# Optimization experiments

Hardware: AMD Instinct MI355X
Metric: run time of the kernel (lower is better)

Reference implementation:

```python
import jax, jax.numpy as jnp
import numpy as np

DIM = 1024
N_SRC = 4096
N_TGT = 4096


def setup_inputs() -> dict:
    key = jax.random.key(0)
    ks = jax.random.split(key, 7)
    scale = 1.0 / np.sqrt(DIM)
    return {
        "source": jax.random.normal(ks[0], (N_SRC, DIM), dtype=jnp.float32),
        "target": jax.random.normal(ks[1], (N_TGT, DIM), dtype=jnp.float32),
        "W_src": jax.random.uniform(ks[2], (DIM, DIM), minval=-scale, maxval=scale, dtype=jnp.float32),
        "b_src": jax.random.uniform(ks[3], (DIM,), minval=-scale, maxval=scale, dtype=jnp.float32),
        "W_tgt": jax.random.uniform(ks[4], (DIM, DIM), minval=-scale, maxval=scale, dtype=jnp.float32),
        "b_tgt": jax.random.uniform(ks[5], (DIM,), minval=-scale, maxval=scale, dtype=jnp.float32),
        "temperature": jnp.array(1.0, dtype=jnp.float32),
    }


def reference(source, target, W_src, b_src, W_tgt, b_tgt, temperature):
    # Linear projections (torch Linear: x @ W.T + b)
    sp = source @ W_src.T + b_src            # [N, d]
    tp = target @ W_tgt.T + b_tgt            # [M, d]
    sq_s = jnp.sum(sp * sp, axis=-1, keepdims=True)   # [N, 1]
    sq_t = jnp.sum(tp * tp, axis=-1)                  # [M]
    d2 = sq_s + sq_t[None, :] - 2.0 * (sp @ tp.T)     # [N, M]
    cost = jnp.sqrt(jnp.maximum(d2, 0.0))
    # Softmin-style kernel, row-normalized over target entries
    K = jnp.exp(-cost / temperature)
    K = K / jnp.sum(K, axis=1, keepdims=True)
    aligned_source = K @ target                       # [N, d]
    return aligned_source, K
```

## Files before the change

kernel.cpp:

```cpp
#include <hip/hip_runtime.h>
#include <stdint.h>

#define DIM  1024
#define NSRC 4096
#define NTGT 4096

typedef __bf16 bf16_t;
typedef bf16_t bf16x8 __attribute__((ext_vector_type(8)));
typedef float  fx4    __attribute__((ext_vector_type(4)));

static __device__ __forceinline__ unsigned short f2bf(float f) {
  union { float f; uint32_t u; } v; v.f = f;
  return (unsigned short)((v.u + 0x7FFFu + ((v.u >> 16) & 1u)) >> 16);
}
static __device__ __forceinline__ float bf2f(unsigned short h) {
  union { uint32_t u; float f; } v; v.u = ((uint32_t)h) << 16;
  return v.f;
}

static __device__ __forceinline__ void gl_lds16(const unsigned short* g, unsigned short* l) {
  __builtin_amdgcn_global_load_lds(
      (__attribute__((address_space(1))) const void*)g,
      (__attribute__((address_space(3))) void*)l, 16, 0, 0);
}


__global__ void k_convert_all(const float* __restrict__ s, const float* __restrict__ t,
                              const float* __restrict__ w0, const float* __restrict__ w1,
                              unsigned short* __restrict__ sb, unsigned short* __restrict__ tb,
                              unsigned short* __restrict__ wb0, unsigned short* __restrict__ wb1) {
  int b = blockIdx.x;
  const float* in; unsigned short* out; int idx;
  if (b < 4096)      { in = s;  out = sb;  idx = b * 256 + threadIdx.x; }
  else if (b < 8192) { in = t;  out = tb;  idx = (b - 4096) * 256 + threadIdx.x; }
  else if (b < 9216) { in = w0; out = wb0; idx = (b - 8192) * 256 + threadIdx.x; }
  else               { in = w1; out = wb1; idx = (b - 9216) * 256 + threadIdx.x; }
  float4 v = ((const float4*)in)[idx];
  ushort4 o;
  o.x = f2bf(v.x); o.y = f2bf(v.y); o.z = f2bf(v.z); o.w = f2bf(v.w);
  ((ushort4*)out)[idx] = o;
}

__global__ void k_transpose_bf16(const float* __restrict__ in, unsigned short* __restrict__ out,
                                 int R, int C) {
  __shared__ unsigned short tile[32][33];
  int c0 = blockIdx.x * 32, r0 = blockIdx.y * 32;
  int tx = threadIdx.x, ty = threadIdx.y;
  for (int i = ty; i < 32; i += 8) {
    int row = r0 + i;
    int p = row & 63;
    int tr = (row & ~63) | ((p >> 2) | ((p & 3) << 4));
    tile[i][tx] = f2bf(in[(size_t)tr * C + c0 + tx]);
  }
  __syncthreads();
  for (int i = ty; i < 32; i += 8)
    out[(size_t)(c0 + i) * R + r0 + tx] = tile[tx][i];
}

__global__ void k_finalize_aligned(const float* __restrict__ P, float* __restrict__ aligned,
                                   const float* __restrict__ rs) {
  const int b = blockIdx.x;
  const int lane = threadIdx.x & 63, w = threadIdx.x >> 6;
  const int src = ((lane & 15) << 2) | (lane >> 4);
  const size_t stride = (size_t)NSRC * DIM;
#pragma unroll
  for (int it = 0; it < 4; ++it) {
    int idx = b * 16 + w * 4 + it;
    size_t base = (size_t)idx * 64;
    float r = 1.0f / rs[idx >> 4];
    float v = (P[base + lane] + P[base + stride + lane]) * r;
    aligned[base + lane] = __shfl(v, src, 64);
  }
}

__global__ void k_finalize_K(const unsigned short* __restrict__ Eb, float* __restrict__ Kf,
                             const float* __restrict__ rs) {
  const int b = blockIdx.x;
  const int lane = threadIdx.x & 63, w = threadIdx.x >> 6;
  const int src = ((lane & 15) << 2) | (lane >> 4);
#pragma unroll
  for (int it = 0; it < 8; ++it) {
    int idx = b * 32 + w * 8 + it;
    size_t base = (size_t)idx * 64;
    float r = 1.0f / rs[idx >> 6];
    float v = bf2f(Eb[base + lane]) * r;
    Kf[base + lane] = __shfl(v, src, 64);
  }
}

template <int EPI>
__global__ void __launch_bounds__(256)
k_gemm(const unsigned short* __restrict__ A0, const unsigned short* __restrict__ B0,
       const unsigned short* __restrict__ A1, const unsigned short* __restrict__ B1,
       int N, int K,
       const float* __restrict__ bias0, const float* __restrict__ bias1,
       unsigned short* __restrict__ Cb0, unsigned short* __restrict__ Cb1,
       float* __restrict__ Cf,
       const float* __restrict__ sqs, const float* __restrict__ sqt,
       const float* __restrict__ tempPtr,
       float* __restrict__ red0, float* __restrict__ red1,
       int KS) {
  __shared__ unsigned short ldsA[128 * 32];
  __shared__ unsigned short ldsB[128 * 32];
  __shared__ float rsum[128];

  const unsigned short* A = A0;
  const unsigned short* B = B0;
  const float* bias = bias0;
  unsigned short* Cb = Cb0;
  float* red = red0;
  int k0 = 0, k1 = K;
  if constexpr (EPI == 0) {
    if (blockIdx.z) { A = A1; B = B1; bias = bias1; Cb = Cb1; red = red1; }
  }
  if constexpr (EPI == 3) { k0 = blockIdx.z * KS; k1 = k0 + KS; }

  const int m0 = blockIdx.y * 128;
  const int n0 = blockIdx.x * 128;
  const int tid  = threadIdx.x;
  const int lane = tid & 63;
  const int wv   = tid >> 6;
  const int wm   = wv >> 1, wn = wv & 1;

  const int c0    = wv * 2;
  const int srow  = lane >> 2;
  const int skoff = (lane & 3) * 8;
  const unsigned short* ag[2]; const unsigned short* bg[2];
  unsigned short* la[2]; unsigned short* lb[2];
#pragma unroll
  for (int j = 0; j < 2; ++j) {
    int c = c0 + j;
    ag[j] = A + (size_t)(m0 + c * 16 + srow) * K + skoff;
    bg[j] = B + (size_t)(n0 + c * 16 + srow) * K + skoff;
    la[j] = ldsA + c * 512;
    lb[j] = ldsB + c * 512;
  }

  const fx4 fzero = {0.f, 0.f, 0.f, 0.f};
  fx4 acc[4][4];
#pragma unroll
  for (int i = 0; i < 4; ++i)
#pragma unroll
    for (int j = 0; j < 4; ++j) acc[i][j] = fzero;

  const int frow = lane & 15;
  const int kq   = lane >> 4;
  const int aoff = (wm * 64 + frow) * 32 + kq * 8;
  const int boff = (wn * 64 + frow) * 32 + kq * 8;

  for (int ko = k0; ko < k1; ko += 32) {
    gl_lds16(ag[0] + ko, la[0]);
    gl_lds16(ag[1] + ko, la[1]);
    gl_lds16(bg[0] + ko, lb[0]);
    gl_lds16(bg[1] + ko, lb[1]);
    __syncthreads();
    bf16x8 af[4], bfr[4];
#pragma unroll
    for (int t = 0; t < 4; ++t) af[t]  = *(const bf16x8*)(ldsA + aoff + t * 512);
#pragma unroll
    for (int t = 0; t < 4; ++t) bfr[t] = *(const bf16x8*)(ldsB + boff + t * 512);
#pragma unroll
    for (int i = 0; i < 4; ++i)
#pragma unroll
      for (int j = 0; j < 4; ++j)
        acc[i][j] = __builtin_amdgcn_mfma_f32_16x16x32_bf16(af[i], bfr[j], acc[i][j], 0, 0, 0);
    __syncthreads();
  }

  const int gcol0 = n0 + wn * 64 + frow;
  const int scol  = n0 + wn * 64 + frow * 4;

  if constexpr (EPI == 0) {
    if (tid < 128) rsum[tid] = 0.f;
    __syncthreads();
#pragma unroll
    for (int i = 0; i < 4; ++i)
#pragma unroll
      for (int r = 0; r < 4; ++r) {
        const int lrow = wm * 64 + kq * 4 + i * 16 + r;
        const int gm   = m0 + lrow;
        float racc = 0.f;
        ushort4 o;
        unsigned short* op = (unsigned short*)&o;
#pragma unroll
        for (int j = 0; j < 4; ++j) {
          float e = acc[i][j][r] + bias[gcol0 + j * 16];
          unsigned short eb = f2bf(e);
          op[j] = eb;
          float ev = bf2f(eb);
          racc += ev * ev;
        }
        *(ushort4*)(Cb + (size_t)gm * N + scol) = o;
        racc += __shfl_xor(racc, 1, 64);
        racc += __shfl_xor(racc, 2, 64);
        racc += __shfl_xor(racc, 4, 64);
        racc += __shfl_xor(racc, 8, 64);
        if (frow == 0) atomicAdd(&rsum[lrow], racc);
      }
    __syncthreads();
    if (tid < 128) atomicAdd(&red[m0 + tid], rsum[tid]);
  } else {
    float* Pz = Cf + (size_t)blockIdx.z * NSRC * DIM;
#pragma unroll
    for (int i = 0; i < 4; ++i)
#pragma unroll
      for (int r = 0; r < 4; ++r) {
        const int gm = m0 + wm * 64 + kq * 4 + i * 16 + r;
        float4 v = make_float4(acc[i][0][r], acc[i][1][r], acc[i][2][r], acc[i][3][r]);
        *(float4*)(Pz + (size_t)gm * N + scol) = v;
      }
  }
}

__global__ void __launch_bounds__(512, 2)
k_score256(const unsigned short* __restrict__ A, const unsigned short* __restrict__ B,
           unsigned short* __restrict__ Eb,
           const float* __restrict__ sqs, const float* __restrict__ sqt,
           const float* __restrict__ tempPtr, float* __restrict__ rsums) {
  __shared__ unsigned short ldsA[32768];
  __shared__ unsigned short ldsB[32768];

  const int tid = threadIdx.x;
  const int lane = tid & 63, w = tid >> 6;
  const int wm = w >> 2, wn = w & 3;
  const int fr = lane & 15, kq = lane >> 4;
  const int m0 = blockIdx.y * 256, n0 = blockIdx.x * 256;

  const int rin = lane >> 2;
  const int cs  = ((lane & 3) * 8) ^ ((lane >> 5) ? 16 : 0);
  const size_t aoff0 = (size_t)(m0 + w * 16 + rin) * DIM + cs;
  const size_t aoff1 = (size_t)(m0 + (8 + w) * 16 + rin) * DIM + cs;
  const size_t boff0 = (size_t)(n0 + w * 16 + rin) * DIM + cs;
  const size_t boff1 = (size_t)(n0 + (8 + w) * 16 + rin) * DIM + cs;

  const int roA = fr * 32 + ((kq * 8) ^ ((fr & 8) ? 16 : 0));

#define STAGE_A(buf, ksb, kk) do { \
    gl_lds16(A + aoff0 + (kk) + (ksb) * 32, ldsA + (buf) * 16384 + (ksb) * 8192 + w * 512); \
    gl_lds16(A + aoff1 + (kk) + (ksb) * 32, ldsA + (buf) * 16384 + (ksb) * 8192 + (8 + w) * 512); \
  } while (0)
#define STAGE_B(buf, ksb, kk) do { \
    gl_lds16(B + boff0 + (kk) + (ksb) * 32, ldsB + (buf) * 16384 + (ksb) * 8192 + w * 512); \
    gl_lds16(B + boff1 + (kk) + (ksb) * 32, ldsB + (buf) * 16384 + (ksb) * 8192 + (8 + w) * 512); \
  } while (0)

  const fx4 fz = {0.f, 0.f, 0.f, 0.f};
  fx4 acc[8][4];
#pragma unroll
  for (int i = 0; i < 8; ++i)
#pragma unroll
    for (int j = 0; j < 4; ++j) acc[i][j] = fz;

  bf16x8 a[8], b0v, b1v;

#define LDA8(buf, ks) do { _Pragma("unroll") \
    for (int i = 0; i < 8; ++i) \
      a[i] = *(const bf16x8*)(ldsA + (buf) * 16384 + (ks) * 8192 + (wm * 8 + i) * 512 + roA); \
  } while (0)
#define LDB2(buf, ks, jh) do { \
    b0v = *(const bf16x8*)(ldsB + (buf) * 16384 + (ks) * 8192 + (wn * 4 + (jh) * 2) * 512 + roA); \
    b1v = *(const bf16x8*)(ldsB + (buf) * 16384 + (ks) * 8192 + (wn * 4 + (jh) * 2 + 1) * 512 + roA); \
  } while (0)
#define MFMA16(jh) do { _Pragma("unroll") \
    for (int i = 0; i < 8; ++i) { \
      acc[i][(jh) * 2]     = __builtin_amdgcn_mfma_f32_16x16x32_bf16(a[i], b0v, acc[i][(jh) * 2], 0, 0, 0); \
      acc[i][(jh) * 2 + 1] = __builtin_amdgcn_mfma_f32_16x16x32_bf16(a[i], b1v, acc[i][(jh) * 2 + 1], 0, 0, 0); \
    } } while (0)
#define BAR()   __builtin_amdgcn_s_barrier()
#define SB0()   __builtin_amdgcn_sched_barrier(0)
#define LGKM0() asm volatile("s_waitcnt lgkmcnt(0)" ::: "memory")
#define VM6()   asm volatile("s_waitcnt vmcnt(6)" ::: "memory")

  STAGE_A(0, 0, 0);  STAGE_B(0, 0, 0);  STAGE_A(0, 1, 0);  STAGE_B(0, 1, 0);
  STAGE_A(1, 0, 64); STAGE_B(1, 0, 64); STAGE_A(1, 1, 64);
  VM6();
  SB0(); BAR();

#pragma unroll 1
  for (int it = 0; it < 8; ++it) {
    const int kk1 = it * 128 + 64;
    const int kk2 = (it * 128 + 128) & (DIM - 1);
    const int kk3 = (it * 128 + 192) & (DIM - 1);
    LDA8(0, 0); LDB2(0, 0, 0); STAGE_B(1, 1, kk1);
    SB0(); BAR(); LGKM0();
    __builtin_amdgcn_s_setprio(1); MFMA16(0); __builtin_amdgcn_s_setprio(0);
    SB0(); BAR();
    LDB2(0, 0, 1); STAGE_A(0, 0, kk2);
    SB0(); BAR(); LGKM0();
    __builtin_amdgcn_s_setprio(1); MFMA16(1); __builtin_amdgcn_s_setprio(0);
    SB0(); BAR();
    LDA8(0, 1); LDB2(0, 1, 0); STAGE_B(0, 0, kk2);
    SB0(); BAR(); LGKM0();
    __builtin_amdgcn_s_setprio(1); MFMA16(0); __builtin_amdgcn_s_setprio(0);
    SB0(); BAR();
    LDB2(0, 1, 1); STAGE_A(0, 1, kk2);
    SB0(); BAR(); LGKM0();
    __builtin_amdgcn_s_setprio(1); MFMA16(1); __builtin_amdgcn_s_setprio(0);
    VM6();
    SB0(); BAR();
    LDA8(1, 0); LDB2(1, 0, 0); STAGE_B(0, 1, kk2);
    SB0(); BAR(); LGKM0();
    __builtin_amdgcn_s_setprio(1); MFMA16(0); __builtin_amdgcn_s_setprio(0);
    SB0(); BAR();
    LDB2(1, 0, 1); STAGE_A(1, 0, kk3);
    SB0(); BAR(); LGKM0();
    __builtin_amdgcn_s_setprio(1); MFMA16(1); __builtin_amdgcn_s_setprio(0);
    SB0(); BAR();
    LDA8(1, 1); LDB2(1, 1, 0); STAGE_B(1, 0, kk3);
    SB0(); BAR(); LGKM0();
    __builtin_amdgcn_s_setprio(1); MFMA16(0); __builtin_amdgcn_s_setprio(0);
    SB0(); BAR();
    LDB2(1, 1, 1); STAGE_A(1, 1, kk3);
    SB0(); BAR(); LGKM0();
    __builtin_amdgcn_s_setprio(1); MFMA16(1); __builtin_amdgcn_s_setprio(0);
    VM6();
    SB0(); BAR();
  }
  asm volatile("s_waitcnt vmcnt(0)" ::: "memory");
  __syncthreads();

  const float invT = 1.0f / tempPtr[0];
  const int gcol0 = n0 + wn * 64 + fr;
  const int scol  = n0 + wn * 64 + fr * 4;
#pragma unroll
  for (int i = 0; i < 8; ++i)
#pragma unroll
    for (int r = 0; r < 4; ++r) {
      const int lrow = wm * 128 + i * 16 + kq * 4 + r;
      const int gm = m0 + lrow;
      const float si = sqs[gm];
      float racc = 0.f;
      ushort4 o; unsigned short* op = (unsigned short*)&o;
#pragma unroll
      for (int j = 0; j < 4; ++j) {
        float d2 = si + sqt[gcol0 + j * 16] - 2.0f * acc[i][j][r];
        float c = sqrtf(fmaxf(d2, 0.0f));
        unsigned short eb = f2bf(__expf(-c * invT));
        op[j] = eb;
        racc += bf2f(eb);
      }
      *(ushort4*)(Eb + (size_t)gm * NTGT + scol) = o;
      racc += __shfl_xor(racc, 1, 64);
      racc += __shfl_xor(racc, 2, 64);
      racc += __shfl_xor(racc, 4, 64);
      racc += __shfl_xor(racc, 8, 64);
      if (fr == 0) atomicAdd(&rsums[gm], racc);
    }
#undef STAGE_A
#undef STAGE_B
#undef LDA8
#undef LDB2
#undef MFMA16
#undef BAR
#undef SB0
#undef LGKM0
#undef VM6
}

extern "C" void kernel_launch(void* const* d_in, const int* in_sizes, int n_in,
                              void* d_out, int out_size, void* d_ws, size_t ws_size,
                              hipStream_t stream) {
  const float* source = (const float*)d_in[0];
  const float* target = (const float*)d_in[1];
  const float* W_src  = (const float*)d_in[2];
  const float* b_src  = (const float*)d_in[3];
  const float* W_tgt  = (const float*)d_in[4];
  const float* b_tgt  = (const float*)d_in[5];
  const float* temp   = (const float*)d_in[6];

  float* out     = (float*)d_out;
  float* aligned = out;
  float* Kout    = out + (size_t)NSRC * DIM;
  float* parts   = Kout;

  char* ws = (char*)d_ws;
  unsigned short* src_b  = (unsigned short*)(ws + 0);
  unsigned short* tgt_b  = (unsigned short*)(ws + 8388608);
  unsigned short* Wsrc_b = (unsigned short*)(ws + 16777216);
  unsigned short* Wtgt_b = (unsigned short*)(ws + 18874368);
  unsigned short* sp_b   = (unsigned short*)(ws + 20971520);
  unsigned short* tp_b   = (unsigned short*)(ws + 29360128);
  unsigned short* tgtT_b = (unsigned short*)(ws + 37748736);
  unsigned short* E_b    = (unsigned short*)(ws + 46137344);
  float* sq_s  = (float*)(ws + 79691776);
  float* sq_t  = (float*)(ws + 79708160);
  float* rsums = (float*)(ws + 79724544);

  hipMemsetAsync(sq_s, 0, 3 * NSRC * sizeof(float), stream);

  k_convert_all<<<10240, 256, 0, stream>>>(source, target, W_src, W_tgt,
                                           src_b, tgt_b, Wsrc_b, Wtgt_b);
  k_transpose_bf16<<<dim3(DIM / 32, NTGT / 32), dim3(32, 8), 0, stream>>>(target, tgtT_b, NTGT, DIM);

  k_gemm<0><<<dim3(DIM / 128, NSRC / 128, 2), 256, 0, stream>>>(
      src_b, Wsrc_b, tgt_b, Wtgt_b, DIM, DIM, b_src, b_tgt, sp_b, tp_b,
      nullptr, nullptr, nullptr, nullptr, sq_s, sq_t, 0);

  k_score256<<<dim3(NTGT / 256, NSRC / 256), 512, 0, stream>>>(
      sp_b, tp_b, E_b, sq_s, sq_t, temp, rsums);

  k_gemm<3><<<dim3(DIM / 128, NSRC / 128, 2), 256, 0, stream>>>(
      E_b, tgtT_b, nullptr, nullptr, DIM, NTGT, nullptr, nullptr, nullptr, nullptr,
      parts, nullptr, nullptr, nullptr, nullptr, nullptr, NTGT / 2);

  k_finalize_aligned<<<4096, 256, 0, stream>>>(parts, aligned, rsums);
  k_finalize_K<<<8192, 256, 0, stream>>>(E_b, Kout, rsums);
}
```

Before: 296.9 us.

## Generalize 256-tile pipelined kernel to projection and aligned GEMMs with 4-way split-K

Replaces the simple 128x128 single-buffered GEMM used for the linear projections and the K@target product with a templated version of the software-pipelined 256x256 score kernel, parameterized by epilogue and leading dimension. The aligned GEMM now uses 4-way split-K over 1024-wide chunks, and the finalize kernel sums four partials. This aims for higher MFMA utilization and data reuse. In exchange it adds partial-buffer traffic and leaves the projection GEMM with fewer blocks than CUs.

```diff
diff --git a/kernel.cpp b/kernel.cpp
--- a/kernel.cpp
+++ b/kernel.cpp
@@ -68,7 +68,8 @@
     int idx = b * 16 + w * 4 + it;
     size_t base = (size_t)idx * 64;
     float r = 1.0f / rs[idx >> 4];
-    float v = (P[base + lane] + P[base + stride + lane]) * r;
+    float v = (P[base + lane] + P[base + stride + lane] +
+               P[base + 2 * stride + lane] + P[base + 3 * stride + lane]) * r;
     aligned[base + lane] = __shfl(v, src, 64);
   }
 }
@@ -88,137 +89,28 @@
   }
 }
 
-template <int EPI>
-__global__ void __launch_bounds__(256)
-k_gemm(const unsigned short* __restrict__ A0, const unsigned short* __restrict__ B0,
-       const unsigned short* __restrict__ A1, const unsigned short* __restrict__ B1,
-       int N, int K,
-       const float* __restrict__ bias0, const float* __restrict__ bias1,
-       unsigned short* __restrict__ Cb0, unsigned short* __restrict__ Cb1,
-       float* __restrict__ Cf,
-       const float* __restrict__ sqs, const float* __restrict__ sqt,
-       const float* __restrict__ tempPtr,
-       float* __restrict__ red0, float* __restrict__ red1,
-       int KS) {
-  __shared__ unsigned short ldsA[128 * 32];
-  __shared__ unsigned short ldsB[128 * 32];
-  __shared__ float rsum[128];
+template <int EPI, int LDK>
+__global__ void __launch_bounds__(512, 2)
+k_tile256(const unsigned short* __restrict__ A0, const unsigned short* __restrict__ B0,
+          const unsigned short* __restrict__ A1, const unsigned short* __restrict__ B1,
+          const float* __restrict__ bias0, const float* __restrict__ bias1,
+          unsigned short* __restrict__ Cb0, unsigned short* __restrict__ Cb1,
+          unsigned short* __restrict__ Eb, float* __restrict__ Cf,
+          const float* __restrict__ sqs, const float* __restrict__ sqt,
+          const float* __restrict__ tempPtr,
+          float* __restrict__ red0, float* __restrict__ red1) {
+  __shared__ unsigned short ldsA[32768];
+  __shared__ unsigned short ldsB[32768];
 
   const unsigned short* A = A0;
   const unsigned short* B = B0;
   const float* bias = bias0;
   unsigned short* Cb = Cb0;
   float* red = red0;
-  int k0 = 0, k1 = K;
   if constexpr (EPI == 0) {
     if (blockIdx.z) { A = A1; B = B1; bias = bias1; Cb = Cb1; red = red1; }
   }
-  if constexpr (EPI == 3) { k0 = blockIdx.z * KS; k1 = k0 + KS; }
-
-  const int m0 = blockIdx.y * 128;
-  const int n0 = blockIdx.x * 128;
-  const int tid  = threadIdx.x;
-  const int lane = tid & 63;
-  const int wv   = tid >> 6;
-  const int wm   = wv >> 1, wn = wv & 1;
-
-  const int c0    = wv * 2;
-  const int srow  = lane >> 2;
-  const int skoff = (lane & 3) * 8;
-  const unsigned short* ag[2]; const unsigned short* bg[2];
-  unsigned short* la[2]; unsigned short* lb[2];
-#pragma unroll
-  for (int j = 0; j < 2; ++j) {
-    int c = c0 + j;
-    ag[j] = A + (size_t)(m0 + c * 16 + srow) * K + skoff;
-    bg[j] = B + (size_t)(n0 + c * 16 + srow) * K + skoff;
-    la[j] = ldsA + c * 512;
-    lb[j] = ldsB + c * 512;
-  }
-
-  const fx4 fzero = {0.f, 0.f, 0.f, 0.f};
-  fx4 acc[4][4];
-#pragma unroll
-  for (int i = 0; i < 4; ++i)
-#pragma unroll
-    for (int j = 0; j < 4; ++j) acc[i][j] = fzero;
-
-  const int frow = lane & 15;
-  const int kq   = lane >> 4;
-  const int aoff = (wm * 64 + frow) * 32 + kq * 8;
-  const int boff = (wn * 64 + frow) * 32 + kq * 8;
-
-  for (int ko = k0; ko < k1; ko += 32) {
-    gl_lds16(ag[0] + ko, la[0]);
-    gl_lds16(ag[1] + ko, la[1]);
-    gl_lds16(bg[0] + ko, lb[0]);
-    gl_lds16(bg[1] + ko, lb[1]);
-    __syncthreads();
-    bf16x8 af[4], bfr[4];
-#pragma unroll
-    for (int t = 0; t < 4; ++t) af[t]  = *(const bf16x8*)(ldsA + aoff + t * 512);
-#pragma unroll
-    for (int t = 0; t < 4; ++t) bfr[t] = *(const bf16x8*)(ldsB + boff + t * 512);
-#pragma unroll
-    for (int i = 0; i < 4; ++i)
-#pragma unroll
-      for (int j = 0; j < 4; ++j)
-        acc[i][j] = __builtin_amdgcn_mfma_f32_16x16x32_bf16(af[i], bfr[j], acc[i][j], 0, 0, 0);
-    __syncthreads();
-  }
-
-  const int gcol0 = n0 + wn * 64 + frow;
-  const int scol  = n0 + wn * 64 + frow * 4;
-
-  if constexpr (EPI == 0) {
-    if (tid < 128) rsum[tid] = 0.f;
-    __syncthreads();
-#pragma unroll
-    for (int i = 0; i < 4; ++i)
-#pragma unroll
-      for (int r = 0; r < 4; ++r) {
-        const int lrow = wm * 64 + kq * 4 + i * 16 + r;
-        const int gm   = m0 + lrow;
-        float racc = 0.f;
-        ushort4 o;
-        unsigned short* op = (unsigned short*)&o;
-#pragma unroll
-        for (int j = 0; j < 4; ++j) {
-          float e = acc[i][j][r] + bias[gcol0 + j * 16];
-          unsigned short eb = f2bf(e);
-          op[j] = eb;
-          float ev = bf2f(eb);
-          racc += ev * ev;
-        }
-        *(ushort4*)(Cb + (size_t)gm * N + scol) = o;
-        racc += __shfl_xor(racc, 1, 64);
-        racc += __shfl_xor(racc, 2, 64);
-        racc += __shfl_xor(racc, 4, 64);
-        racc += __shfl_xor(racc, 8, 64);
-        if (frow == 0) atomicAdd(&rsum[lrow], racc);
-      }
-    __syncthreads();
-    if (tid < 128) atomicAdd(&red[m0 + tid], rsum[tid]);
-  } else {
-    float* Pz = Cf + (size_t)blockIdx.z * NSRC * DIM;
-#pragma unroll
-    for (int i = 0; i < 4; ++i)
-#pragma unroll
-      for (int r = 0; r < 4; ++r) {
-        const int gm = m0 + wm * 64 + kq * 4 + i * 16 + r;
-        float4 v = make_float4(acc[i][0][r], acc[i][1][r], acc[i][2][r], acc[i][3][r]);
-        *(float4*)(Pz + (size_t)gm * N + scol) = v;
-      }
-  }
-}
-
-__global__ void __launch_bounds__(512, 2)
-k_score256(const unsigned short* __restrict__ A, const unsigned short* __restrict__ B,
-           unsigned short* __restrict__ Eb,
-           const float* __restrict__ sqs, const float* __restrict__ sqt,
-           const float* __restrict__ tempPtr, float* __restrict__ rsums) {
-  __shared__ unsigned short ldsA[32768];
-  __shared__ unsigned short ldsB[32768];
+  if constexpr (EPI == 3) { A += blockIdx.z * 1024; B += blockIdx.z * 1024; }
 
   const int tid = threadIdx.x;
   const int lane = tid & 63, w = tid >> 6;
@@ -228,10 +120,10 @@
 
   const int rin = lane >> 2;
   const int cs  = ((lane & 3) * 8) ^ ((lane >> 5) ? 16 : 0);
-  const size_t aoff0 = (size_t)(m0 + w * 16 + rin) * DIM + cs;
-  const size_t aoff1 = (size_t)(m0 + (8 + w) * 16 + rin) * DIM + cs;
-  const size_t boff0 = (size_t)(n0 + w * 16 + rin) * DIM + cs;
-  const size_t boff1 = (size_t)(n0 + (8 + w) * 16 + rin) * DIM + cs;
+  const size_t aoff0 = (size_t)(m0 + w * 16 + rin) * LDK + cs;
+  const size_t aoff1 = (size_t)(m0 + (8 + w) * 16 + rin) * LDK + cs;
+  const size_t boff0 = (size_t)(n0 + w * 16 + rin) * LDK + cs;
+  const size_t boff1 = (size_t)(n0 + (8 + w) * 16 + rin) * LDK + cs;
 
   const int roA = fr * 32 + ((kq * 8) ^ ((fr & 8) ? 16 : 0));
 
@@ -279,8 +171,8 @@
 #pragma unroll 1
   for (int it = 0; it < 8; ++it) {
     const int kk1 = it * 128 + 64;
-    const int kk2 = (it * 128 + 128) & (DIM - 1);
-    const int kk3 = (it * 128 + 192) & (DIM - 1);
+    const int kk2 = (it * 128 + 128) & 1023;
+    const int kk3 = (it * 128 + 192) & 1023;
     LDA8(0, 0); LDB2(0, 0, 0); STAGE_B(1, 1, kk1);
     SB0(); BAR(); LGKM0();
     __builtin_amdgcn_s_setprio(1); MFMA16(0); __builtin_amdgcn_s_setprio(0);
@@ -319,33 +211,68 @@
   asm volatile("s_waitcnt vmcnt(0)" ::: "memory");
   __syncthreads();
 
-  const float invT = 1.0f / tempPtr[0];
   const int gcol0 = n0 + wn * 64 + fr;
   const int scol  = n0 + wn * 64 + fr * 4;
-#pragma unroll
-  for (int i = 0; i < 8; ++i)
-#pragma unroll
-    for (int r = 0; r < 4; ++r) {
-      const int lrow = wm * 128 + i * 16 + kq * 4 + r;
-      const int gm = m0 + lrow;
-      const float si = sqs[gm];
-      float racc = 0.f;
-      ushort4 o; unsigned short* op = (unsigned short*)&o;
-#pragma unroll
-      for (int j = 0; j < 4; ++j) {
-        float d2 = si + sqt[gcol0 + j * 16] - 2.0f * acc[i][j][r];
-        float c = sqrtf(fmaxf(d2, 0.0f));
-        unsigned short eb = f2bf(__expf(-c * invT));
-        op[j] = eb;
-        racc += bf2f(eb);
+
+  if constexpr (EPI == 0) {
+#pragma unroll
+    for (int i = 0; i < 8; ++i)
+#pragma unroll
+      for (int r = 0; r < 4; ++r) {
+        const int gm = m0 + wm * 128 + i * 16 + kq * 4 + r;
+        float racc = 0.f;
+        ushort4 o; unsigned short* op = (unsigned short*)&o;
+#pragma unroll
+        for (int j = 0; j < 4; ++j) {
+          float e = acc[i][j][r] + bias[gcol0 + j * 16];
+          unsigned short eb = f2bf(e);
+          op[j] = eb;
+          float ev = bf2f(eb);
+          racc += ev * ev;
+        }
+        *(ushort4*)(Cb + (size_t)gm * DIM + scol) = o;
+        racc += __shfl_xor(racc, 1, 64);
+        racc += __shfl_xor(racc, 2, 64);
+        racc += __shfl_xor(racc, 4, 64);
+        racc += __shfl_xor(racc, 8, 64);
+        if (fr == 0) atomicAdd(&red[gm], racc);
       }
-      *(ushort4*)(Eb + (size_t)gm * NTGT + scol) = o;
-      racc += __shfl_xor(racc, 1, 64);
-      racc += __shfl_xor(racc, 2, 64);
-      racc += __shfl_xor(racc, 4, 64);
-      racc += __shfl_xor(racc, 8, 64);
-      if (fr == 0) atomicAdd(&rsums[gm], racc);
-    }
+  } else if constexpr (EPI == 1) {
+    const float invT = 1.0f / tempPtr[0];
+#pragma unroll
+    for (int i = 0; i < 8; ++i)
+#pragma unroll
+      for (int r = 0; r < 4; ++r) {
+        const int gm = m0 + wm * 128 + i * 16 + kq * 4 + r;
+        const float si = sqs[gm];
+        float racc = 0.f;
+        ushort4 o; unsigned short* op = (unsigned short*)&o;
+#pragma unroll
+        for (int j = 0; j < 4; ++j) {
+          float d2 = si + sqt[gcol0 + j * 16] - 2.0f * acc[i][j][r];
+          float c = sqrtf(fmaxf(d2, 0.0f));
+          unsigned short eb = f2bf(__expf(-c * invT));
+          op[j] = eb;
+          racc += bf2f(eb);
+        }
+        *(ushort4*)(Eb + (size_t)gm * NTGT + scol) = o;
+        racc += __shfl_xor(racc, 1, 64);
+        racc += __shfl_xor(racc, 2, 64);
+        racc += __shfl_xor(racc, 4, 64);
+        racc += __shfl_xor(racc, 8, 64);
+        if (fr == 0) atomicAdd(&red[gm], racc);
+      }
+  } else {
+    float* Pz = Cf + (size_t)blockIdx.z * NSRC * DIM;
+#pragma unroll
+    for (int i = 0; i < 8; ++i)
+#pragma unroll
+      for (int r = 0; r < 4; ++r) {
+        const int gm = m0 + wm * 128 + i * 16 + kq * 4 + r;
+        float4 v = make_float4(acc[i][0][r], acc[i][1][r], acc[i][2][r], acc[i][3][r]);
+        *(float4*)(Pz + (size_t)gm * DIM + scol) = v;
+      }
+  }
 #undef STAGE_A
 #undef STAGE_B
 #undef LDA8
@@ -392,16 +319,17 @@
                                            src_b, tgt_b, Wsrc_b, Wtgt_b);
   k_transpose_bf16<<<dim3(DIM / 32, NTGT / 32), dim3(32, 8), 0, stream>>>(target, tgtT_b, NTGT, DIM);
 
-  k_gemm<0><<<dim3(DIM / 128, NSRC / 128, 2), 256, 0, stream>>>(
-      src_b, Wsrc_b, tgt_b, Wtgt_b, DIM, DIM, b_src, b_tgt, sp_b, tp_b,
-      nullptr, nullptr, nullptr, nullptr, sq_s, sq_t, 0);
-
-  k_score256<<<dim3(NTGT / 256, NSRC / 256), 512, 0, stream>>>(
-      sp_b, tp_b, E_b, sq_s, sq_t, temp, rsums);
-
-  k_gemm<3><<<dim3(DIM / 128, NSRC / 128, 2), 256, 0, stream>>>(
-      E_b, tgtT_b, nullptr, nullptr, DIM, NTGT, nullptr, nullptr, nullptr, nullptr,
-      parts, nullptr, nullptr, nullptr, nullptr, nullptr, NTGT / 2);
+  k_tile256<0, DIM><<<dim3(DIM / 256, NSRC / 256, 2), 512, 0, stream>>>(
+      src_b, Wsrc_b, tgt_b, Wtgt_b, b_src, b_tgt, sp_b, tp_b,
+      nullptr, nullptr, nullptr, nullptr, nullptr, sq_s, sq_t);
+
+  k_tile256<1, DIM><<<dim3(NTGT / 256, NSRC / 256, 1), 512, 0, stream>>>(
+      sp_b, tp_b, nullptr, nullptr, nullptr, nullptr, nullptr, nullptr,
+      E_b, nullptr, sq_s, sq_t, temp, rsums, nullptr);
+
+  k_tile256<3, NTGT><<<dim3(DIM / 256, NSRC / 256, 4), 512, 0, stream>>>(
+      E_b, tgtT_b, nullptr, nullptr, nullptr, nullptr, nullptr, nullptr,
+      nullptr, parts, nullptr, nullptr, nullptr, nullptr, nullptr);
 
   k_finalize_aligned<<<4096, 256, 0, stream>>>(parts, aligned, rsums);
   k_finalize_K<<<8192, 256, 0, stream>>>(E_b, Kout, rsums);
```

Result: faster. 280.2 us (-5.6%).
